# Optimization experiments

Measured on AMD Instinct MI355X. Metric: run time of the kernel, lower is better.

Reference implementation:

```python
import jax, jax.numpy as jnp
import numpy as np

JACCARD_THRESH = 0.5
NEGPOS_RATIO = 3
V0, V1 = 0.1, 0.2  # SSD encoding variances


def setup_inputs() -> dict:
    key = jax.random.key(0)
    k1, k2, k3, k4, k5, k6, k7 = jax.random.split(key, 7)
    B, P, C, O = 128, 8732, 21, 16
    loc_data = jax.random.normal(k1, (B, P, 4), dtype=jnp.float32)
    conf_data = jax.random.normal(k2, (B, P, C), dtype=jnp.float32)
    # default boxes in center form (cx, cy, w, h), all in [0,1]
    cxcy = jax.random.uniform(k3, (P, 2), minval=0.05, maxval=0.95)
    wh = jax.random.uniform(k4, (P, 2), minval=0.05, maxval=0.6)
    dbox_list = jnp.concatenate([cxcy, wh], axis=1).astype(jnp.float32)
    # ground-truth boxes in corner form with guaranteed positive extent
    tl = jax.random.uniform(k5, (B, O, 2), minval=0.0, maxval=0.6)
    sz = jax.random.uniform(k6, (B, O, 2), minval=0.05, maxval=0.35)
    labels = jax.random.randint(k7, (B, O, 1), 0, C - 1).astype(jnp.float32)
    targets = jnp.concatenate([tl, tl + sz, labels], axis=2)
    return {"loc_data": loc_data, "conf_data": conf_data,
            "dbox_list": dbox_list, "targets": targets}


def _match_one(truths, labels, dbox):
    """SSD match for one image. truths:[O,4] corner, labels:[O], dbox:[P,4] center."""
    pf = jnp.concatenate([dbox[:, :2] - dbox[:, 2:] * 0.5,
                          dbox[:, :2] + dbox[:, 2:] * 0.5], axis=1)  # point form [P,4]
    lt = jnp.maximum(truths[:, None, :2], pf[None, :, :2])
    rb = jnp.minimum(truths[:, None, 2:], pf[None, :, 2:])
    whi = jnp.clip(rb - lt, 0.0)
    inter = whi[..., 0] * whi[..., 1]                                # [O,P]
    area_t = (truths[:, 2] - truths[:, 0]) * (truths[:, 3] - truths[:, 1])
    area_p = dbox[:, 2] * dbox[:, 3]
    ov = inter / (area_t[:, None] + area_p[None, :] - inter)         # jaccard [O,P]
    best_prior_idx = jnp.argmax(ov, axis=1)                          # [O]
    bto = jnp.max(ov, axis=0)                                        # [P]
    bti = jnp.argmax(ov, axis=0)                                     # [P]
    bto = bto.at[best_prior_idx].set(2.0)
    O = truths.shape[0]
    bti = jax.lax.fori_loop(0, O, lambda j, b: b.at[best_prior_idx[j]].set(j), bti)
    matched = truths[bti]                                            # [P,4]
    conf = labels[bti].astype(jnp.int32) + 1
    conf = jnp.where(bto < JACCARD_THRESH, 0, conf)
    g_cxcy = ((matched[:, :2] + matched[:, 2:]) * 0.5 - dbox[:, :2]) / (V0 * dbox[:, 2:])
    g_wh = jnp.log((matched[:, 2:] - matched[:, :2]) / dbox[:, 2:]) / V1
    return jnp.concatenate([g_cxcy, g_wh], axis=1), conf


def reference(loc_data, conf_data, dbox_list, targets):
    B, P, C = conf_data.shape
    loc_t, conf_t = jax.vmap(_match_one, in_axes=(0, 0, None))(
        targets[..., :4], targets[..., 4], dbox_list)
    pos = conf_t > 0                                                  # [B,P]
    # smooth L1 (beta=1), summed over positives
    ad = jnp.abs(loc_data - loc_t)
    sl1 = jnp.where(ad < 1.0, 0.5 * ad * ad, ad - 0.5)
    loss_l = jnp.sum(jnp.where(pos[..., None], sl1, 0.0))
    # per-prior cross entropy
    logp = jax.nn.log_softmax(conf_data, axis=-1)
    ce = -jnp.take_along_axis(logp, conf_t[..., None], axis=-1)[..., 0]  # [B,P]
    # hard negative mining via double argsort (rank in descending order)
    ce_neg = jnp.where(pos, 0.0, ce)
    loss_idx = jnp.argsort(-ce_neg, axis=1)
    idx_rank = jnp.argsort(loss_idx, axis=1)
    num_pos = jnp.sum(pos, axis=1, keepdims=True)
    num_neg = jnp.minimum(num_pos * NEGPOS_RATIO, P)
    neg = idx_rank < num_neg
    sel = pos | neg
    loss_c = jnp.sum(jnp.where(sel, ce, 0.0))
    N = jnp.sum(num_pos).astype(loc_data.dtype)
    return jnp.stack([loss_l / N, loss_c / N])
```

## Files before the change

### kernel.cpp

```cpp
#include <hip/hip_runtime.h>
#include <cstddef>

#define Bn 128
#define Pn 8732
#define Cn 21
#define On 16
#define MAGIC 0x13579BDFu

__device__ __forceinline__ void argmax_combine(float& v, int& p, float v2, int p2) {
  if (v2 > v || (v2 == v && p2 < p)) { v = v2; p = p2; }
}

__device__ __forceinline__ float sl1_enc(float4 lv, float4 d,
                                         float t0, float t1, float t2, float t3) {
  float g0 = ((t0 + t2) * 0.5f - d.x) / (0.1f * d.z);
  float g1 = ((t1 + t3) * 0.5f - d.y) / (0.1f * d.w);
  float g2 = __logf((t2 - t0) / d.z) / 0.2f;
  float g3 = __logf((t3 - t1) / d.w) / 0.2f;
  float r = 0.f, a;
  a = fabsf(lv.x - g0); r += (a < 1.f) ? 0.5f * a * a : a - 0.5f;
  a = fabsf(lv.y - g1); r += (a < 1.f) ? 0.5f * a * a : a - 0.5f;
  a = fabsf(lv.z - g2); r += (a < 1.f) ? 0.5f * a * a : a - 0.5f;
  a = fabsf(lv.w - g3); r += (a < 1.f) ? 0.5f * a * a : a - 0.5f;
  return r;
}

__global__ __launch_bounds__(256) void stream_kernel(
    const float* __restrict__ conf, const float* __restrict__ dbox,
    const float* __restrict__ targets,
    float* __restrict__ ce0, unsigned char* __restrict__ pack,
    unsigned long long* __restrict__ keys) {
  const int wb = threadIdx.x >> 6, lane = threadIdx.x & 63;
  const int wave_g = blockIdx.x * 4 + wb;
  const int b = wave_g & 127;
  const int cg = wave_g >> 7;

  __shared__ float4 s_row4[4][336];
  __shared__ float s_tt[4][On * 5];
  __shared__ float s_ar[4][On];

  for (int i = lane; i < On * 5; i += 64)
    s_tt[wb][i] = targets[(size_t)b * On * 5 + i];
  if (lane < On) {
    float x1 = targets[(size_t)b * On * 5 + lane * 5 + 0];
    float y1 = targets[(size_t)b * On * 5 + lane * 5 + 1];
    float x2 = targets[(size_t)b * On * 5 + lane * 5 + 2];
    float y2 = targets[(size_t)b * On * 5 + lane * 5 + 3];
    s_ar[wb][lane] = (x2 - x1) * (y2 - y1);
  }

  float bestv[On]; int bestp[On];
  #pragma unroll
  for (int j = 0; j < On; j++) { bestv[j] = -1.0f; bestp[j] = 0x7fffffff; }

  #pragma unroll
  for (int i = 0; i < 5; i++) {
    const int ci = cg + 32 * i;
    if (ci >= 137) break;
    const int p0 = ci * 64;
    const int rows = min(64, Pn - p0);
    const int n4 = rows * Cn / 4;

    const float4* src = (const float4*)(conf + ((size_t)b * Pn + p0) * Cn);
    float4 v0, v1, v2, v3, v4, v5;
    if (lane < n4)        v0 = src[lane];
    if (lane + 64 < n4)   v1 = src[lane + 64];
    if (lane + 128 < n4)  v2 = src[lane + 128];
    if (lane + 192 < n4)  v3 = src[lane + 192];
    if (lane + 256 < n4)  v4 = src[lane + 256];
    if (lane + 320 < n4)  v5 = src[lane + 320];
    if (lane < n4)        s_row4[wb][lane] = v0;
    if (lane + 64 < n4)   s_row4[wb][lane + 64] = v1;
    if (lane + 128 < n4)  s_row4[wb][lane + 128] = v2;
    if (lane + 192 < n4)  s_row4[wb][lane + 192] = v3;
    if (lane + 256 < n4)  s_row4[wb][lane + 256] = v4;
    if (lane + 320 < n4)  s_row4[wb][lane + 320] = v5;

    if (lane < rows) {
      const int p = p0 + lane;
      const float* x = (const float*)s_row4[wb] + lane * Cn;
      float m = x[0];
      #pragma unroll
      for (int q = 1; q < Cn; q++) m = fmaxf(m, x[q]);
      float s = 0.0f;
      #pragma unroll
      for (int q = 0; q < Cn; q++) s += __expf(x[q] - m);
      float lse = m + __logf(s);
      ce0[(size_t)b * Pn + p] = lse - x[0];

      float4 d = ((const float4*)dbox)[p];
      float px1 = d.x - d.z * 0.5f, py1 = d.y - d.w * 0.5f;
      float px2 = d.x + d.z * 0.5f, py2 = d.y + d.w * 0.5f;
      float ap = d.z * d.w;
      float mv = -1.0f; int mj = 0;
      #pragma unroll
      for (int j = 0; j < On; j++) {
        float lx = fmaxf(s_tt[wb][j*5+0], px1);
        float ly = fmaxf(s_tt[wb][j*5+1], py1);
        float rx = fminf(s_tt[wb][j*5+2], px2);
        float ry = fminf(s_tt[wb][j*5+3], py2);
        float w = fmaxf(rx - lx, 0.0f), h = fmaxf(ry - ly, 0.0f);
        float inter = w * h;
        float ov = __fdividef(inter, s_ar[wb][j] + ap - inter);
        if (ov > bestv[j]) { bestv[j] = ov; bestp[j] = p; }
        if (ov > mv) { mv = ov; mj = j; }
      }
      pack[(size_t)b * Pn + p] =
          (unsigned char)(mj | ((mv >= 0.5f) ? 16 : 0));
    }
  }

  #pragma unroll
  for (int j = 0; j < On; j++) {
    float v = bestv[j]; int p = bestp[j];
    #pragma unroll
    for (int off = 32; off; off >>= 1) {
      float v2 = __shfl_down(v, off);
      int p2 = __shfl_down(p, off);
      argmax_combine(v, p, v2, p2);
    }
    if (lane == 0) {
      unsigned long long key;
      if (v < 0.0f) key = 0xC000000000000000ull;
      else key = (((unsigned long long)(__float_as_uint(v) | 0xC0000000u)) << 32)
               | (unsigned long long)(0xFFFFFFFFu - (unsigned)p);
      atomicMax(&keys[b * On + j], key);
    }
  }
}

__global__ __launch_bounds__(1024) void reduce_kernel(
    const float* __restrict__ loc, const float* __restrict__ conf,
    const float* __restrict__ dbox, const float* __restrict__ targets,
    const float* __restrict__ ce0, const unsigned char* __restrict__ pack,
    const unsigned long long* __restrict__ keys,
    unsigned int* __restrict__ res, float* __restrict__ out) {
  const int b = blockIdx.x;
  const int tid = threadIdx.x;
  const int wave = tid >> 6, lane = tid & 63;

  __shared__ float s_t[On * 5];
  __shared__ int s_bp[On];
  __shared__ unsigned s_bm[273];
  __shared__ unsigned hist[256 * 16];
  __shared__ unsigned s_col[256];
  __shared__ unsigned s_cand[64];
  __shared__ float s_redf[2][16];
  __shared__ int s_redi[16];
  __shared__ unsigned s_prefix;
  __shared__ int s_kk;
  __shared__ int s_cnt;
  __shared__ int s_cc;
  __shared__ int s_np;
  __shared__ float s_floc, s_fcep;

  if (tid < On * 5) s_t[tid] = targets[(size_t)b * On * 5 + tid];
  if (tid < 273) s_bm[tid] = 0;
  __syncthreads();
  if (tid < On) {
    int bp = (int)(0xFFFFFFFFu - (unsigned)(keys[b * On + tid] & 0xFFFFFFFFull));
    s_bp[tid] = bp;
    atomicOr(&s_bm[bp >> 5], 1u << (bp & 31));
  }
  __syncthreads();

  if (wave == 0) {
    float f_loc = 0.f, f_cep = 0.f;
    const bool valid = lane < On;
    const int p = valid ? s_bp[lane] : 0;
    bool dup = false;
    if (valid)
      for (int j2 = lane + 1; j2 < On; j2++) dup |= (s_bp[j2] == p);
    if (valid && !dup) {
      const float* row = conf + ((size_t)b * Pn + p) * Cn;
      float m = row[0];
      #pragma unroll
      for (int q = 1; q < Cn; q++) m = fmaxf(m, row[q]);
      float s = 0.f;
      #pragma unroll
      for (int q = 0; q < Cn; q++) s += __expf(row[q] - m);
      const float lse = m + __logf(s);
      const int c = (int)s_t[lane * 5 + 4] + 1;
      f_cep = lse - row[c];
      const float4 d = ((const float4*)dbox)[p];
      const float4 lv = ((const float4*)loc)[(size_t)b * Pn + p];
      f_loc = sl1_enc(lv, d, s_t[lane*5+0], s_t[lane*5+1],
                             s_t[lane*5+2], s_t[lane*5+3]);
    }
    #pragma unroll
    for (int off = 32; off; off >>= 1) {
      f_loc += __shfl_down(f_loc, off);
      f_cep += __shfl_down(f_cep, off);
    }
    if (lane == 0) { s_floc = f_loc; s_fcep = f_cep; }
  }

  float ce_r[9];
  float my_loc = 0.0f, my_cep = 0.0f; int my_np = 0;
  #pragma unroll
  for (int sI = 0; sI < 9; sI++) {
    ce_r[sI] = 0.0f;
    const int p = tid + 1024 * sI;
    if (p < Pn) {
      unsigned char pk = pack[(size_t)b * Pn + p];
      float c0 = ce0[(size_t)b * Pn + p];
      const unsigned forced = (s_bm[p >> 5] >> (p & 31)) & 1u;
      const int posb = (pk >> 4);
      const int pos = posb | (int)forced;
      ce_r[sI] = pos ? 0.0f : c0;
      if (pos) my_np++;
      if (posb && !forced) {
        const int bt = pk & 15;
        const float* t = &s_t[bt * 5];
        int c = (int)t[4] + 1;
        const float* row = conf + ((size_t)b * Pn + p) * Cn;
        my_cep += c0 + row[0] - row[c];
        float4 d = ((const float4*)dbox)[p];
        float4 ld = ((const float4*)loc)[(size_t)b * Pn + p];
        my_loc += sl1_enc(ld, d, t[0], t[1], t[2], t[3]);
      }
    }
  }

  {
    int np = my_np;
    #pragma unroll
    for (int off = 32; off; off >>= 1) np += __shfl_down(np, off);
    if (lane == 0) s_redi[wave] = np;
  }
  __syncthreads();
  if (tid == 0) {
    int np = 0;
    #pragma unroll
    for (int w = 0; w < 16; w++) np += s_redi[w];
    s_np = np;
  }
  __syncthreads();

  const int k = min(s_np * 3, Pn);
  unsigned prefix = 0, maskb = 0;
  int kk = k;
  int cntc = Pn;
  for (int shift = 24; shift >= 0; shift -= 8) {
    if (cntc <= 64) break;
    ((uint4*)hist)[tid] = make_uint4(0u, 0u, 0u, 0u);
    __syncthreads();
    #pragma unroll
    for (int sI = 0; sI < 9; sI++) {
      const int p = tid + 1024 * sI;
      if (p < Pn) {
        unsigned u = __float_as_uint(ce_r[sI]);
        if ((u & maskb) == prefix)
          atomicAdd(&hist[(((u >> shift) & 255u) << 4) + (unsigned)wave], 1u);
      }
    }
    __syncthreads();
    if (tid < 256) {
      unsigned c = 0;
      #pragma unroll
      for (int w = 0; w < 16; w++) c += hist[(tid << 4) + w];
      s_col[tid] = c;
    }
    __syncthreads();
    if (tid < 64) {
      unsigned c0 = s_col[4 * tid + 0], c1 = s_col[4 * tid + 1];
      unsigned c2 = s_col[4 * tid + 2], c3 = s_col[4 * tid + 3];
      unsigned t0 = c0 + c1 + c2 + c3;
      unsigned S = t0;
      #pragma unroll
      for (int off = 1; off < 64; off <<= 1) {
        unsigned o = __shfl_down(S, off);
        if (tid + off < 64) S += o;
      }
      unsigned Snext = S - t0;
      unsigned s3 = Snext + c3;
      unsigned s2 = s3 + c2;
      unsigned s1 = s2 + c1;
      unsigned s0 = s1 + c0;
      unsigned kk_u = (unsigned)kk;
      int chosen = -1; unsigned snx = 0, cc = 0;
      if (s3 >= kk_u && Snext < kk_u)      { chosen = 3; snx = Snext; cc = c3; }
      else if (s2 >= kk_u && s3 < kk_u)    { chosen = 2; snx = s3;    cc = c2; }
      else if (s1 >= kk_u && s2 < kk_u)    { chosen = 1; snx = s2;    cc = c1; }
      else if (s0 >= kk_u && s1 < kk_u)    { chosen = 0; snx = s1;    cc = c0; }
      if (chosen >= 0) {
        s_prefix = prefix | ((unsigned)(4 * tid + chosen) << shift);
        s_kk = (int)(kk_u - snx);
        s_cnt = (int)cc;
      }
    }
    __syncthreads();
    prefix = s_prefix; kk = s_kk; cntc = s_cnt;
    maskb |= 255u << shift;
  }
  if (maskb != 0xFFFFFFFFu) {
    if (tid == 0) s_cc = 0;
    __syncthreads();
    #pragma unroll
    for (int sI = 0; sI < 9; sI++) {
      const int p = tid + 1024 * sI;
      if (p < Pn) {
        unsigned u = __float_as_uint(ce_r[sI]);
        if ((u & maskb) == prefix) {
          int ix = atomicAdd(&s_cc, 1);
          if (ix < 64) s_cand[ix] = u;
        }
      }
    }
    __syncthreads();
    if (tid < 64) {
      int c = min(s_cc, 64);
      if (tid < c) {
        unsigned v = s_cand[tid];
        int g = 0, e = 0;
        for (int i = 0; i < c; i++) {
          unsigned w = s_cand[i];
          g += (w > v); e += (w == v);
        }
        if (g < kk && kk <= g + e) s_prefix = v;
      }
    }
    __syncthreads();
    prefix = s_prefix;
  }
  float T = __uint_as_float(prefix);

  float sum_gt = 0.0f; int cnt_gt = 0;
  #pragma unroll
  for (int sI = 0; sI < 9; sI++) {
    const int p = tid + 1024 * sI;
    if (p < Pn) {
      float x = ce_r[sI];
      if (x > T) { sum_gt += x; cnt_gt++; }
    }
  }
  #pragma unroll
  for (int off = 32; off; off >>= 1) {
    sum_gt += __shfl_down(sum_gt, off);
    cnt_gt += __shfl_down(cnt_gt, off);
    my_loc += __shfl_down(my_loc, off);
    my_cep += __shfl_down(my_cep, off);
  }
  if (lane == 0) {
    s_redf[0][wave] = my_loc; s_redf[1][wave] = sum_gt + my_cep; s_redi[wave] = cnt_gt;
  }
  __syncthreads();
  if (tid == 0) {
    float ll = s_floc, lc = s_fcep; int cg2 = 0;
    #pragma unroll
    for (int w = 0; w < 16; w++) {
      ll += s_redf[0][w]; lc += s_redf[1][w]; cg2 += s_redi[w];
    }
    lc += (k > 0) ? (float)(k - cg2) * T : 0.0f;
    atomicExch(&res[b * 4 + 0], __float_as_uint(ll));
    atomicExch(&res[b * 4 + 1], __float_as_uint(lc));
    atomicExch(&res[b * 4 + 2], (unsigned)s_np);
    __threadfence();
    atomicExch(&res[b * 4 + 3], MAGIC);
  }

  if (b == 0 && tid < 64) {
    float ll = 0.0f, lc = 0.0f; int np = 0;
    #pragma unroll
    for (int h = 0; h < 2; h++) {
      const int i = tid + 64 * h;
      while (atomicAdd(&res[i * 4 + 3], 0u) != MAGIC) { __builtin_amdgcn_s_sleep(8); }
      ll += __uint_as_float(atomicAdd(&res[i * 4 + 0], 0u));
      lc += __uint_as_float(atomicAdd(&res[i * 4 + 1], 0u));
      np += (int)atomicAdd(&res[i * 4 + 2], 0u);
    }
    #pragma unroll
    for (int off = 32; off; off >>= 1) {
      ll += __shfl_down(ll, off);
      lc += __shfl_down(lc, off);
      np += __shfl_down(np, off);
    }
    if (tid == 0) {
      float fN = (float)np;
      out[0] = ll / fN;
      out[1] = lc / fN;
    }
  }
}

extern "C" void kernel_launch(void* const* d_in, const int* in_sizes, int n_in,
                              void* d_out, int out_size, void* d_ws, size_t ws_size,
                              hipStream_t stream) {
  const float* loc_data  = (const float*)d_in[0];
  const float* conf_data = (const float*)d_in[1];
  const float* dbox      = (const float*)d_in[2];
  const float* targets   = (const float*)d_in[3];
  float* out = (float*)d_out;

  char* ws = (char*)d_ws;
  float* ce0 = (float*)ws;
  unsigned char* pack = (unsigned char*)(ws + (size_t)Bn * Pn * 4);
  unsigned long long* keys =
      (unsigned long long*)(ws + (size_t)Bn * Pn * 5);
  unsigned int* res = (unsigned int*)(ws + (size_t)Bn * Pn * 5 + Bn * On * 8);

  stream_kernel<<<1024, 256, 0, stream>>>(conf_data, dbox, targets, ce0, pack, keys);
  reduce_kernel<<<Bn, 1024, 0, stream>>>(loc_data, conf_data, dbox, targets,
                                         ce0, pack, keys, res, out);
}
```

Before: 202.3 us.

## Double-buffer conf chunks via direct global-to-LDS loads with one-wave blocks

Each wave now runs as its own 64-thread block and streams its conf chunks into two LDS buffers using global_load_lds. The next chunk's load is issued before the current chunk is computed, with hand-placed vmcnt waits and sched barriers. Default-box values are preloaded into registers up front instead of inside each chunk. The goal is to hide HBM latency behind the softmax and IoU math. The manual waitcnt counts are fragile and could race if the compiler emits other vector memory ops in between.

```diff
diff --git a/kernel.cpp b/kernel.cpp
--- a/kernel.cpp
+++ b/kernel.cpp
@@ -6,6 +6,10 @@
 #define Cn 21
 #define On 16
 #define MAGIC 0x13579BDFu
+
+#define SB() __builtin_amdgcn_sched_barrier(0)
+#define VW(n) asm volatile("s_waitcnt vmcnt(" #n ")" ::: "memory")
+#define USE4(v) asm volatile("" :: "v"((v).x), "v"((v).y), "v"((v).z), "v"((v).w))
 
 __device__ __forceinline__ void argmax_combine(float& v, int& p, float v2, int p2) {
   if (v2 > v || (v2 == v && p2 < p)) { v = v2; p = p2; }
@@ -25,60 +29,66 @@
   return r;
 }
 
-__global__ __launch_bounds__(256) void stream_kernel(
+__global__ __launch_bounds__(64) void stream_kernel(
     const float* __restrict__ conf, const float* __restrict__ dbox,
     const float* __restrict__ targets,
     float* __restrict__ ce0, unsigned char* __restrict__ pack,
     unsigned long long* __restrict__ keys) {
-  const int wb = threadIdx.x >> 6, lane = threadIdx.x & 63;
-  const int wave_g = blockIdx.x * 4 + wb;
-  const int b = wave_g & 127;
-  const int cg = wave_g >> 7;
-
-  __shared__ float4 s_row4[4][336];
-  __shared__ float s_tt[4][On * 5];
-  __shared__ float s_ar[4][On];
-
-  for (int i = lane; i < On * 5; i += 64)
-    s_tt[wb][i] = targets[(size_t)b * On * 5 + i];
+  const int lane = threadIdx.x;
+  const int b = blockIdx.x & 127;
+  const int cg = blockIdx.x >> 7;
+
+  __shared__ float4 s_buf[2][336];
+  __shared__ float s_tt[On * 5];
+  __shared__ float s_ar[On];
+
+  const size_t tb = (size_t)b * On * 5;
+  for (int i = lane; i < On * 5; i += 64) s_tt[i] = targets[tb + i];
   if (lane < On) {
-    float x1 = targets[(size_t)b * On * 5 + lane * 5 + 0];
-    float y1 = targets[(size_t)b * On * 5 + lane * 5 + 1];
-    float x2 = targets[(size_t)b * On * 5 + lane * 5 + 2];
-    float y2 = targets[(size_t)b * On * 5 + lane * 5 + 3];
-    s_ar[wb][lane] = (x2 - x1) * (y2 - y1);
-  }
+    float x1 = targets[tb + lane * 5 + 0];
+    float y1 = targets[tb + lane * 5 + 1];
+    float x2 = targets[tb + lane * 5 + 2];
+    float y2 = targets[tb + lane * 5 + 3];
+    s_ar[lane] = (x2 - x1) * (y2 - y1);
+  }
+
+  const int c0 = cg, c1 = cg + 32, c2 = cg + 64, c3 = cg + 96, c4 = cg + 128;
+  const bool has5 = (cg < 9);
+  const bool full5 = (cg < 8);
+
+  float4 d0 = ((const float4*)dbox)[c0 * 64 + lane];
+  float4 d1 = ((const float4*)dbox)[c1 * 64 + lane];
+  float4 d2 = ((const float4*)dbox)[c2 * 64 + lane];
+  float4 d3 = ((const float4*)dbox)[c3 * 64 + lane];
+  float4 d4 = make_float4(0.f, 0.f, 0.f, 0.f);
+  if (has5 && (c4 * 64 + lane) < Pn) d4 = ((const float4*)dbox)[c4 * 64 + lane];
+  USE4(d0); USE4(d1); USE4(d2); USE4(d3); USE4(d4);
 
   float bestv[On]; int bestp[On];
   #pragma unroll
   for (int j = 0; j < On; j++) { bestv[j] = -1.0f; bestp[j] = 0x7fffffff; }
 
-  #pragma unroll
-  for (int i = 0; i < 5; i++) {
-    const int ci = cg + 32 * i;
-    if (ci >= 137) break;
+  auto STAGE = [&](int bi, int ci) {
+    const int p0 = ci * 64;
+    const int n4 = min(64, Pn - p0) * Cn / 4;
+    const float4* src = (const float4*)(conf + ((size_t)b * Pn + p0) * Cn);
+    #pragma unroll
+    for (int k = 0; k < 6; k++) {
+      if (64 * k + lane < n4) {
+        __builtin_amdgcn_global_load_lds(
+            (const __attribute__((address_space(1))) unsigned int*)(src + 64 * k + lane),
+            (__attribute__((address_space(3))) unsigned int*)(&s_buf[bi][64 * k]),
+            16, 0, 0);
+      }
+    }
+  };
+
+  auto COMPUTE = [&](int ci, int bi, float4 d) {
     const int p0 = ci * 64;
     const int rows = min(64, Pn - p0);
-    const int n4 = rows * Cn / 4;
-
-    const float4* src = (const float4*)(conf + ((size_t)b * Pn + p0) * Cn);
-    float4 v0, v1, v2, v3, v4, v5;
-    if (lane < n4)        v0 = src[lane];
-    if (lane + 64 < n4)   v1 = src[lane + 64];
-    if (lane + 128 < n4)  v2 = src[lane + 128];
-    if (lane + 192 < n4)  v3 = src[lane + 192];
-    if (lane + 256 < n4)  v4 = src[lane + 256];
-    if (lane + 320 < n4)  v5 = src[lane + 320];
-    if (lane < n4)        s_row4[wb][lane] = v0;
-    if (lane + 64 < n4)   s_row4[wb][lane + 64] = v1;
-    if (lane + 128 < n4)  s_row4[wb][lane + 128] = v2;
-    if (lane + 192 < n4)  s_row4[wb][lane + 192] = v3;
-    if (lane + 256 < n4)  s_row4[wb][lane + 256] = v4;
-    if (lane + 320 < n4)  s_row4[wb][lane + 320] = v5;
-
     if (lane < rows) {
       const int p = p0 + lane;
-      const float* x = (const float*)s_row4[wb] + lane * Cn;
+      const float* x = (const float*)s_buf[bi] + lane * Cn;
       float m = x[0];
       #pragma unroll
       for (int q = 1; q < Cn; q++) m = fmaxf(m, x[q]);
@@ -88,26 +98,45 @@
       float lse = m + __logf(s);
       ce0[(size_t)b * Pn + p] = lse - x[0];
 
-      float4 d = ((const float4*)dbox)[p];
       float px1 = d.x - d.z * 0.5f, py1 = d.y - d.w * 0.5f;
       float px2 = d.x + d.z * 0.5f, py2 = d.y + d.w * 0.5f;
       float ap = d.z * d.w;
       float mv = -1.0f; int mj = 0;
       #pragma unroll
       for (int j = 0; j < On; j++) {
-        float lx = fmaxf(s_tt[wb][j*5+0], px1);
-        float ly = fmaxf(s_tt[wb][j*5+1], py1);
-        float rx = fminf(s_tt[wb][j*5+2], px2);
-        float ry = fminf(s_tt[wb][j*5+3], py2);
+        float lx = fmaxf(s_tt[j*5+0], px1);
+        float ly = fmaxf(s_tt[j*5+1], py1);
+        float rx = fminf(s_tt[j*5+2], px2);
+        float ry = fminf(s_tt[j*5+3], py2);
         float w = fmaxf(rx - lx, 0.0f), h = fmaxf(ry - ly, 0.0f);
         float inter = w * h;
-        float ov = __fdividef(inter, s_ar[wb][j] + ap - inter);
+        float ov = __fdividef(inter, s_ar[j] + ap - inter);
         if (ov > bestv[j]) { bestv[j] = ov; bestp[j] = p; }
         if (ov > mv) { mv = ov; mj = j; }
       }
       pack[(size_t)b * Pn + p] =
           (unsigned char)(mj | ((mv >= 0.5f) ? 16 : 0));
     }
+  };
+
+  VW(0); SB();
+  STAGE(0, c0); SB();
+  STAGE(1, c1); SB(); VW(6); SB();
+  COMPUTE(c0, 0, d0); SB();
+  STAGE(0, c2); SB(); VW(8); SB();
+  COMPUTE(c1, 1, d1); SB();
+  STAGE(1, c3); SB(); VW(8); SB();
+  COMPUTE(c2, 0, d2); SB();
+  if (has5) {
+    STAGE(0, c4); SB();
+    if (full5) { VW(8); } else { VW(5); }
+    SB();
+    COMPUTE(c3, 1, d3); SB();
+    VW(0); SB();
+    COMPUTE(c4, 0, d4);
+  } else {
+    VW(0); SB();
+    COMPUTE(c3, 1, d3);
   }
 
   #pragma unroll
@@ -399,7 +428,7 @@
       (unsigned long long*)(ws + (size_t)Bn * Pn * 5);
   unsigned int* res = (unsigned int*)(ws + (size_t)Bn * Pn * 5 + Bn * On * 8);
 
-  stream_kernel<<<1024, 256, 0, stream>>>(conf_data, dbox, targets, ce0, pack, keys);
+  stream_kernel<<<4096, 64, 0, stream>>>(conf_data, dbox, targets, ce0, pack, keys);
   reduce_kernel<<<Bn, 1024, 0, stream>>>(loc_data, conf_data, dbox, targets,
                                          ce0, pack, keys, res, out);
 }
```

New measurement: 211.4 us. 4.5% more time.
